# Optimization experiments

Measured on AMD Instinct MI355X. Metric: run time of the kernel, lower is better.

The kernel has to match this reference:

```python
import jax, jax.numpy as jnp
import numpy as np

NUM_ENT = 40000
NUM_REL = 100
EMBED_DIM = 256
FEAT_DIM = 768
BATCH = 32
SEQ_LEN = 3
MASK_POS = 2
EPS = 1e-12


def setup_inputs() -> dict:
    key = jax.random.key(0)
    k1, k2, k3, k4 = jax.random.split(key, 4)
    ent_pkl = jax.random.normal(k1, (NUM_ENT, FEAT_DIM), dtype=jnp.float32)
    other_emb = jax.random.normal(k2, (NUM_ENT + NUM_REL + 3 - NUM_ENT, EMBED_DIM), dtype=jnp.float32)
    proj_W = jax.random.normal(k3, (EMBED_DIM, FEAT_DIM), dtype=jnp.float32) * (1.0 / np.sqrt(FEAT_DIM))
    batch_input_ids = jax.random.randint(k4, (BATCH, SEQ_LEN), 0, NUM_ENT + NUM_REL + 3, dtype=jnp.int64)
    return {
        "ent_pkl": ent_pkl,
        "other_emb": other_emb,
        "proj_W": proj_W,
        "batch_input_ids": batch_input_ids,
        "batch_mask_position": MASK_POS,
    }


def reference(ent_pkl, other_emb, proj_W, batch_input_ids, batch_mask_position):
    # unity embeddings: [other[0], proj(ent_pkl), other[1:]] -> [num_ent+num_rel+3, d]
    ent_proj = ent_pkl @ proj_W.T  # Linear(feat_dim, embed_dim, bias=False)
    unity = jnp.concatenate([other_emb[:1], ent_proj, other_emb[1:]], axis=0)

    mp = int(batch_mask_position)
    # drop the masked slot, keep up to 3 tokens total -> [B, 2]
    query_input = jnp.concatenate(
        [batch_input_ids[:, :mp], batch_input_ids[:, mp + 1:3]], axis=1)
    query_emb = unity[query_input]  # [B, 2, d]
    # F.normalize(dim=-1): x / max(||x||_2, eps)
    norm = jnp.sqrt(jnp.sum(query_emb * query_emb, axis=-1, keepdims=True))
    query_emb = query_emb / jnp.maximum(norm, EPS)
    query_sum = jnp.sum(query_emb, axis=1)  # [B, d]

    E_embed = unity[:NUM_ENT + 1]  # [num_ent+1, d]
    # broadcast L1 distance: [B, num_ent+1]
    score = -jnp.sum(jnp.abs(query_sum[:, None, :] - E_embed[None, :, :]), axis=-1)
    return score
```

## Files before the change

kernel.cpp:

```cpp
#include <hip/hip_runtime.h>
#include <hip/hip_bf16.h>
#include <stdint.h>

#define NE 40000
#define FD 768
#define ED 256
#define NB 32
#define OUTC (NE + 1)

typedef __bf16 bf16x8 __attribute__((ext_vector_type(8)));
typedef float f32x4 __attribute__((ext_vector_type(4)));
typedef float f32x16 __attribute__((ext_vector_type(16)));
typedef _Float16 f16x2 __attribute__((ext_vector_type(2)));
typedef _Float16 f16x4 __attribute__((ext_vector_type(4)));

#define WS_QS 0
#define WS_N01 (32 * 1024)
#define WS_WB (96 * 1024)

__device__ __forceinline__ f16x2 pabs2(f16x2 d) {
    union { f16x2 h; unsigned u; } v; v.h = d; v.u &= 0x7FFF7FFFu; return v.h;
}

__device__ __forceinline__ void gload16(const void* g, void* l) {
    __builtin_amdgcn_global_load_lds(
        (const __attribute__((address_space(1))) unsigned int*)g,
        (__attribute__((address_space(3))) unsigned int*)l, 16, 0, 0);
}

__global__ __launch_bounds__(256) void prep_kernel(
    const float* __restrict__ ent_pkl, const float* __restrict__ W,
    const int* __restrict__ ids, const int* __restrict__ mpos,
    __bf16* __restrict__ Wf, float* __restrict__ n01_raw)
{
    __shared__ f32x4 xs4[FD / 4];
    const int bid = blockIdx.x;
    const int t = threadIdx.x;

    if (bid < 192) {
        const int i = bid * 1024 + t * 4;
        const int r = i / FD, c = i - r * FD;
        float4 v = *(const float4*)(W + i);
        __bf16 o[4] = {(__bf16)v.x, (__bf16)v.y, (__bf16)v.z, (__bf16)v.w};
        const int f = ((r >> 5) * 48 + (c >> 4)) * 64 + (r & 31) + ((c >> 3) & 1) * 32;
        *(ushort4*)(Wf + (size_t)f * 8 + (c & 7)) = *(const ushort4*)o;
        return;
    }

    const int sub = bid - 192;
    const int slot = sub >> 2;
    const int oq = sub & 3;
    const int b = slot >> 1, s = slot & 1;
    const int mp = mpos[0];
    const int col = (s < mp) ? s : s + 1;
    const bool wide = (ids[1] == 0 && ids[3] == 0 && ids[5] == 0);
    const int flat = b * 3 + col;
    const int idx = wide ? ids[flat * 2] : ids[flat];
    if (!(idx >= 1 && idx <= NE)) return;

    if (t < FD / 4) xs4[t] = ((const f32x4*)(ent_pkl + (size_t)(idx - 1) * FD))[t];
    __syncthreads();

    const int l = t & 63, wv = t >> 6;
    const f32x4 x0 = xs4[l], x1 = xs4[l + 64], x2 = xs4[l + 128];
    const int obase = oq * 64 + wv * 16;
#pragma unroll 2
    for (int i = 0; i < 16; ++i) {
        const int o = obase + i;
        const f32x4* wr = (const f32x4*)(W + (size_t)o * FD);
        f32x4 w0 = wr[l], w1 = wr[l + 64], w2 = wr[l + 128];
        float p = w0[0] * x0[0] + w0[1] * x0[1] + w0[2] * x0[2] + w0[3] * x0[3]
                + w1[0] * x1[0] + w1[1] * x1[1] + w1[2] * x1[2] + w1[3] * x1[3]
                + w2[0] * x2[0] + w2[1] * x2[1] + w2[2] * x2[2] + w2[3] * x2[3];
#pragma unroll
        for (int off = 32; off; off >>= 1) p += __shfl_xor(p, off, 64);
        if (l == 0) n01_raw[slot * ED + o] = p;
    }
}

__global__ __launch_bounds__(256) void qsum_kernel(
    const float* __restrict__ other_emb, const float* __restrict__ n01_raw,
    const int* __restrict__ ids, const int* __restrict__ mpos,
    _Float16* __restrict__ qh, float* __restrict__ out)
{
    __shared__ float red[4];
    __shared__ float nshare;
    const int b = blockIdx.x, t = threadIdx.x;
    const int mp = mpos[0];
    const bool wide = (ids[1] == 0 && ids[3] == 0 && ids[5] == 0);

    float q = 0.f;
#pragma unroll
    for (int s = 0; s < 2; ++s) {
        const int col = (s < mp) ? s : s + 1;
        const int flat = b * 3 + col;
        const int idx = wide ? ids[flat * 2] : ids[flat];
        float v;
        if (idx >= 1 && idx <= NE) v = n01_raw[(b * 2 + s) * ED + t];
        else if (idx == 0) v = other_emb[t];
        else v = other_emb[(size_t)(idx - NE) * ED + t];

        float ss = v * v;
#pragma unroll
        for (int o = 32; o > 0; o >>= 1) ss += __shfl_down(ss, o, 64);
        if ((t & 63) == 0) red[t >> 6] = ss;
        __syncthreads();
        if (t == 0) nshare = fmaxf(sqrtf(red[0] + red[1] + red[2] + red[3]), 1e-12f);
        __syncthreads();
        q += v / nshare;
        __syncthreads();
    }
    qh[b * ED + t] = (_Float16)q;

    float d = fabsf(q - other_emb[t]);
#pragma unroll
    for (int o = 32; o > 0; o >>= 1) d += __shfl_down(d, o, 64);
    if ((t & 63) == 0) red[t >> 6] = d;
    __syncthreads();
    if (t == 0) out[(size_t)b * OUTC] = -(red[0] + red[1] + red[2] + red[3]);
}

#define SP 256

__global__ __launch_bounds__(512, 6) void gemm_score_kernel(
    const float* __restrict__ ent_pkl, const __bf16* __restrict__ Wf,
    const _Float16* __restrict__ qh, float* __restrict__ out)
{
    __shared__ __align__(16) unsigned char smem[49152];
    float* Af = (float*)smem;
    _Float16* Sb = (_Float16*)smem;
    _Float16* qL = (_Float16*)(smem + 32768);

    const int t = threadIdx.x;
    const int l = t & 63;
    const int w = t >> 6;
    const int m31 = l & 31;
    const int dh = l >> 5;
    const int e0 = blockIdx.x * 64;

    f32x16 acc0, acc1;
#pragma unroll
    for (int i = 0; i < 16; ++i) { acc0[i] = 0.f; acc1[i] = 0.f; }

    int srow[6], slc[6];
#pragma unroll
    for (int j = 0; j < 6; ++j) {
        const int p = j * 512 + t;
        const int r = p / 48;
        srow[j] = r;
        slc[j] = (p - r * 48) ^ (r & 7);
    }

    const __bf16* bp = Wf + (size_t)w * 24576 + (size_t)l * 8;
    const int sw = m31 & 7;
    const float* a0base = Af + m31 * 192;
    const float* a1base = Af + (32 + m31) * 192;

    for (int q = 0; q < 4; ++q) {
        __syncthreads();
#pragma unroll
        for (int j = 0; j < 6; ++j) {
            gload16(ent_pkl + (size_t)(e0 + srow[j]) * FD + q * 192 + slc[j] * 4,
                    (float*)smem + (size_t)(j * 512 + t) * 4);
        }
        __syncthreads();
        const __bf16* bq = bp + (size_t)q * 12 * 512;
#pragma unroll 4
        for (int c = 0; c < 12; ++c) {
            bf16x8 bv = *(const bf16x8*)(bq + c * 512);
            const int u0 = 4 * c + 2 * dh;
            const int p0 = (u0 ^ sw) * 4, p1 = ((u0 + 1) ^ sw) * 4;
            f32x4 lo0 = *(const f32x4*)(a0base + p0);
            f32x4 hi0 = *(const f32x4*)(a0base + p1);
            f32x4 lo1 = *(const f32x4*)(a1base + p0);
            f32x4 hi1 = *(const f32x4*)(a1base + p1);
            bf16x8 a0, a1;
            a0[0] = (__bf16)lo0[0]; a0[1] = (__bf16)lo0[1]; a0[2] = (__bf16)lo0[2]; a0[3] = (__bf16)lo0[3];
            a0[4] = (__bf16)hi0[0]; a0[5] = (__bf16)hi0[1]; a0[6] = (__bf16)hi0[2]; a0[7] = (__bf16)hi0[3];
            a1[0] = (__bf16)lo1[0]; a1[1] = (__bf16)lo1[1]; a1[2] = (__bf16)lo1[2]; a1[3] = (__bf16)lo1[3];
            a1[4] = (__bf16)hi1[0]; a1[5] = (__bf16)hi1[1]; a1[6] = (__bf16)hi1[2]; a1[7] = (__bf16)hi1[3];
            acc0 = __builtin_amdgcn_mfma_f32_32x32x16_bf16(a0, bv, acc0, 0, 0, 0);
            acc1 = __builtin_amdgcn_mfma_f32_32x32x16_bf16(a1, bv, acc1, 0, 0, 0);
        }
    }

    __syncthreads();
    const int colg = 8 * w + (m31 >> 2);
    const int csub = m31 & 3;
#pragma unroll
    for (int r = 0; r < 16; ++r) {
        const int erow = (r & 3) + 8 * (r >> 2) + 4 * dh;
        const int ph = (((colg ^ (erow & 15)) << 2) | csub);
        Sb[erow * SP + ph] = (_Float16)acc0[r];
        Sb[(32 + erow) * SP + ph] = (_Float16)acc1[r];
    }
    {
        const uint4* qsrc = (const uint4*)qh;
        uint4* qdst = (uint4*)qL;
        qdst[t] = qsrc[t];
        qdst[t + 512] = qsrc[t + 512];
    }
    __syncthreads();

    const int wu = __builtin_amdgcn_readfirstlane(w);
    const f16x4* q0 = (const f16x4*)(qL + (size_t)(4 * wu + 0) * ED);
    const f16x4* q1 = (const f16x4*)(qL + (size_t)(4 * wu + 1) * ED);
    const f16x4* q2 = (const f16x4*)(qL + (size_t)(4 * wu + 2) * ED);
    const f16x4* q3 = (const f16x4*)(qL + (size_t)(4 * wu + 3) * ED);
    const int swl = l & 15;
    const _Float16* xbase = Sb + (size_t)l * SP;

    float s0 = 0.f, s1 = 0.f, s2 = 0.f, s3 = 0.f;
    for (int cb = 0; cb < 8; ++cb) {
        f16x2 t0 = {0, 0}, t1 = {0, 0}, t2 = {0, 0}, t3 = {0, 0};
#pragma unroll
        for (int ci = 0; ci < 8; ++ci) {
            const int c = cb * 8 + ci;
            f16x4 xv = *(const f16x4*)(xbase + ((c ^ swl) << 2));
            f16x2 xlo = __builtin_shufflevector(xv, xv, 0, 1);
            f16x2 xhi = __builtin_shufflevector(xv, xv, 2, 3);
            f16x4 qa = q0[c], qb = q1[c], qc = q2[c], qd = q3[c];
            t0 = t0 + pabs2(__builtin_shufflevector(qa, qa, 0, 1) - xlo);
            t0 = t0 + pabs2(__builtin_shufflevector(qa, qa, 2, 3) - xhi);
            t1 = t1 + pabs2(__builtin_shufflevector(qb, qb, 0, 1) - xlo);
            t1 = t1 + pabs2(__builtin_shufflevector(qb, qb, 2, 3) - xhi);
            t2 = t2 + pabs2(__builtin_shufflevector(qc, qc, 0, 1) - xlo);
            t2 = t2 + pabs2(__builtin_shufflevector(qc, qc, 2, 3) - xhi);
            t3 = t3 + pabs2(__builtin_shufflevector(qd, qd, 0, 1) - xlo);
            t3 = t3 + pabs2(__builtin_shufflevector(qd, qd, 2, 3) - xhi);
        }
        s0 += (float)t0[0] + (float)t0[1];
        s1 += (float)t1[0] + (float)t1[1];
        s2 += (float)t2[0] + (float)t2[1];
        s3 += (float)t3[0] + (float)t3[1];
    }
    float* ob = out + 1 + e0 + l;
    __builtin_nontemporal_store(-s0, ob + (size_t)(4 * wu + 0) * OUTC);
    __builtin_nontemporal_store(-s1, ob + (size_t)(4 * wu + 1) * OUTC);
    __builtin_nontemporal_store(-s2, ob + (size_t)(4 * wu + 2) * OUTC);
    __builtin_nontemporal_store(-s3, ob + (size_t)(4 * wu + 3) * OUTC);
}

extern "C" void kernel_launch(void* const* d_in, const int* in_sizes, int n_in,
                              void* d_out, int out_size, void* d_ws, size_t ws_size,
                              hipStream_t stream) {
    const float* ent_pkl = (const float*)d_in[0];
    const float* other_emb = (const float*)d_in[1];
    const float* proj_W = (const float*)d_in[2];
    const int* ids = (const int*)d_in[3];
    const int* mpos = (const int*)d_in[4];
    float* out = (float*)d_out;

    _Float16* qh = (_Float16*)((char*)d_ws + WS_QS);
    float* n01_raw = (float*)((char*)d_ws + WS_N01);
    __bf16* Wf = (__bf16*)((char*)d_ws + WS_WB);

    prep_kernel<<<448, 256, 0, stream>>>(ent_pkl, proj_W, ids, mpos, Wf, n01_raw);
    qsum_kernel<<<NB, 256, 0, stream>>>(other_emb, n01_raw, ids, mpos, qh, out);
    gemm_score_kernel<<<NE / 64, 512, 0, stream>>>(ent_pkl, Wf, qh, out);
}
```

Baseline: 245.4 us.

## Double-buffer bf16 A tiles in register-staged pipeline and restructure projection prep

The GEMM kernel now loads ent_pkl rows into registers and converts them to bf16 once per element before writing them into one of two ping-pong LDS buffers in MFMA fragment layout. The next K-slab's global loads are issued before the current slab's MFMAs, and it takes a single barrier per step instead of two around direct global-to-LDS loads. This removes the repeated fp32-to-bf16 conversions in the inner loop and halves LDS footprint per stage, at the cost of more register pressure and eight smaller K steps. The prep kernel's query-projection path is also rewritten so each thread computes one output dot product serially, with fewer blocks launched.

```diff
diff --git a/kernel.cpp b/kernel.cpp
--- a/kernel.cpp
+++ b/kernel.cpp
@@ -8,6 +8,7 @@
 #define NB 32
 #define OUTC (NE + 1)
 
+typedef __bf16 bf16x4 __attribute__((ext_vector_type(4)));
 typedef __bf16 bf16x8 __attribute__((ext_vector_type(8)));
 typedef float f32x4 __attribute__((ext_vector_type(4)));
 typedef float f32x16 __attribute__((ext_vector_type(16)));
@@ -22,18 +23,11 @@
     union { f16x2 h; unsigned u; } v; v.h = d; v.u &= 0x7FFF7FFFu; return v.h;
 }
 
-__device__ __forceinline__ void gload16(const void* g, void* l) {
-    __builtin_amdgcn_global_load_lds(
-        (const __attribute__((address_space(1))) unsigned int*)g,
-        (__attribute__((address_space(3))) unsigned int*)l, 16, 0, 0);
-}
-
 __global__ __launch_bounds__(256) void prep_kernel(
     const float* __restrict__ ent_pkl, const float* __restrict__ W,
     const int* __restrict__ ids, const int* __restrict__ mpos,
     __bf16* __restrict__ Wf, float* __restrict__ n01_raw)
 {
-    __shared__ f32x4 xs4[FD / 4];
     const int bid = blockIdx.x;
     const int t = threadIdx.x;
 
@@ -47,34 +41,36 @@
         return;
     }
 
-    const int sub = bid - 192;
-    const int slot = sub >> 2;
-    const int oq = sub & 3;
-    const int b = slot >> 1, s = slot & 1;
+    const int pb = bid - 192;
     const int mp = mpos[0];
-    const int col = (s < mp) ? s : s + 1;
     const bool wide = (ids[1] == 0 && ids[3] == 0 && ids[5] == 0);
-    const int flat = b * 3 + col;
-    const int idx = wide ? ids[flat * 2] : ids[flat];
-    if (!(idx >= 1 && idx <= NE)) return;
-
-    if (t < FD / 4) xs4[t] = ((const f32x4*)(ent_pkl + (size_t)(idx - 1) * FD))[t];
-    __syncthreads();
-
-    const int l = t & 63, wv = t >> 6;
-    const f32x4 x0 = xs4[l], x1 = xs4[l + 64], x2 = xs4[l + 128];
-    const int obase = oq * 64 + wv * 16;
-#pragma unroll 2
-    for (int i = 0; i < 16; ++i) {
-        const int o = obase + i;
-        const f32x4* wr = (const f32x4*)(W + (size_t)o * FD);
-        f32x4 w0 = wr[l], w1 = wr[l + 64], w2 = wr[l + 128];
-        float p = w0[0] * x0[0] + w0[1] * x0[1] + w0[2] * x0[2] + w0[3] * x0[3]
-                + w1[0] * x1[0] + w1[1] * x1[1] + w1[2] * x1[2] + w1[3] * x1[3]
-                + w2[0] * x2[0] + w2[1] * x2[1] + w2[2] * x2[2] + w2[3] * x2[3];
-#pragma unroll
-        for (int off = 32; off; off >>= 1) p += __shfl_xor(p, off, 64);
-        if (l == 0) n01_raw[slot * ED + o] = p;
+
+#pragma unroll
+    for (int sub = 0; sub < 2; ++sub) {
+        const int id = sub * 256 + t;
+        const int o = id & 7;
+        const int s = id >> 3;
+        const int b = s >> 1, sq = s & 1;
+        const int col = (sq < mp) ? sq : sq + 1;
+        const int flat = b * 3 + col;
+        const int idx = wide ? ids[flat * 2] : ids[flat];
+        if (!(idx >= 1 && idx <= NE)) continue;
+
+        const f32x4* wr = (const f32x4*)(W + (size_t)(pb * 8 + o) * FD);
+        const f32x4* xr = (const f32x4*)(ent_pkl + (size_t)(idx - 1) * FD);
+        float a0 = 0.f, a1 = 0.f, a2 = 0.f, a3 = 0.f;
+#pragma unroll 4
+        for (int k = 0; k < FD / 4; k += 4) {
+            f32x4 w0 = wr[k], x0 = xr[k];
+            f32x4 w1 = wr[k + 1], x1 = xr[k + 1];
+            f32x4 w2 = wr[k + 2], x2 = xr[k + 2];
+            f32x4 w3 = wr[k + 3], x3 = xr[k + 3];
+            a0 += w0[0]*x0[0] + w0[1]*x0[1] + w0[2]*x0[2] + w0[3]*x0[3];
+            a1 += w1[0]*x1[0] + w1[1]*x1[1] + w1[2]*x1[2] + w1[3]*x1[3];
+            a2 += w2[0]*x2[0] + w2[1]*x2[1] + w2[2]*x2[2] + w2[3]*x2[3];
+            a3 += w3[0]*x3[0] + w3[1]*x3[1] + w3[2]*x3[2] + w3[3]*x3[3];
+        }
+        n01_raw[s * ED + pb * 8 + o] = (a0 + a1) + (a2 + a3);
     }
 }
 
@@ -121,13 +117,25 @@
 }
 
 #define SP 256
+#define ABUF 12288
+
+__device__ __forceinline__ void write3(__bf16* B, const int* woff, const f32x4* st) {
+#pragma unroll
+    for (int j = 0; j < 3; ++j) {
+        bf16x4 v;
+        v[0] = (__bf16)st[j][0]; v[1] = (__bf16)st[j][1];
+        v[2] = (__bf16)st[j][2]; v[3] = (__bf16)st[j][3];
+        *(bf16x4*)((char*)B + woff[j]) = v;
+    }
+}
 
 __global__ __launch_bounds__(512, 6) void gemm_score_kernel(
     const float* __restrict__ ent_pkl, const __bf16* __restrict__ Wf,
     const _Float16* __restrict__ qh, float* __restrict__ out)
 {
     __shared__ __align__(16) unsigned char smem[49152];
-    float* Af = (float*)smem;
+    __bf16* A0 = (__bf16*)smem;
+    __bf16* A1 = (__bf16*)(smem + ABUF);
     _Float16* Sb = (_Float16*)smem;
     _Float16* qL = (_Float16*)(smem + 32768);
 
@@ -142,45 +150,47 @@
 #pragma unroll
     for (int i = 0; i < 16; ++i) { acc0[i] = 0.f; acc1[i] = 0.f; }
 
-    int srow[6], slc[6];
-#pragma unroll
-    for (int j = 0; j < 6; ++j) {
-        const int p = j * 512 + t;
-        const int r = p / 48;
-        srow[j] = r;
-        slc[j] = (p - r * 48) ^ (r & 7);
+    const int srow = t >> 3, sseg = t & 7;
+    const float* abase = ent_pkl + (size_t)(e0 + srow) * FD + sseg * 12;
+    int woff[3];
+#pragma unroll
+    for (int j = 0; j < 3; ++j) {
+        const int k0 = sseg * 12 + 4 * j;
+        const int unit = ((k0 >> 4) * 2 + ((k0 >> 3) & 1)) * 64 + srow;
+        woff[j] = unit * 16 + (k0 & 7) * 2;
     }
 
     const __bf16* bp = Wf + (size_t)w * 24576 + (size_t)l * 8;
-    const int sw = m31 & 7;
-    const float* a0base = Af + m31 * 192;
-    const float* a1base = Af + (32 + m31) * 192;
-
-    for (int q = 0; q < 4; ++q) {
-        __syncthreads();
-#pragma unroll
-        for (int j = 0; j < 6; ++j) {
-            gload16(ent_pkl + (size_t)(e0 + srow[j]) * FD + q * 192 + slc[j] * 4,
-                    (float*)smem + (size_t)(j * 512 + t) * 4);
-        }
-        __syncthreads();
-        const __bf16* bq = bp + (size_t)q * 12 * 512;
-#pragma unroll 4
-        for (int c = 0; c < 12; ++c) {
+
+    f32x4 st[3];
+    st[0] = *(const f32x4*)(abase + 0);
+    st[1] = *(const f32x4*)(abase + 4);
+    st[2] = *(const f32x4*)(abase + 8);
+    write3(A0, woff, st);
+    __syncthreads();
+
+    for (int p = 0; p < 8; ++p) {
+        const __bf16* Ab = (p & 1) ? A1 : A0;
+        __bf16* An = (p & 1) ? A0 : A1;
+        if (p < 7) {
+            const float* np = abase + (p + 1) * 96;
+            st[0] = *(const f32x4*)(np + 0);
+            st[1] = *(const f32x4*)(np + 4);
+            st[2] = *(const f32x4*)(np + 8);
+        }
+        const __bf16* bq = bp + (size_t)p * 6 * 512;
+#pragma unroll
+        for (int c = 0; c < 6; ++c) {
             bf16x8 bv = *(const bf16x8*)(bq + c * 512);
-            const int u0 = 4 * c + 2 * dh;
-            const int p0 = (u0 ^ sw) * 4, p1 = ((u0 + 1) ^ sw) * 4;
-            f32x4 lo0 = *(const f32x4*)(a0base + p0);
-            f32x4 hi0 = *(const f32x4*)(a0base + p1);
-            f32x4 lo1 = *(const f32x4*)(a1base + p0);
-            f32x4 hi1 = *(const f32x4*)(a1base + p1);
-            bf16x8 a0, a1;
-            a0[0] = (__bf16)lo0[0]; a0[1] = (__bf16)lo0[1]; a0[2] = (__bf16)lo0[2]; a0[3] = (__bf16)lo0[3];
-            a0[4] = (__bf16)hi0[0]; a0[5] = (__bf16)hi0[1]; a0[6] = (__bf16)hi0[2]; a0[7] = (__bf16)hi0[3];
-            a1[0] = (__bf16)lo1[0]; a1[1] = (__bf16)lo1[1]; a1[2] = (__bf16)lo1[2]; a1[3] = (__bf16)lo1[3];
-            a1[4] = (__bf16)hi1[0]; a1[5] = (__bf16)hi1[1]; a1[6] = (__bf16)hi1[2]; a1[7] = (__bf16)hi1[3];
+            const __bf16* fa = Ab + ((c * 2 + dh) * 64 + m31) * 8;
+            bf16x8 a0 = *(const bf16x8*)(fa);
+            bf16x8 a1 = *(const bf16x8*)(fa + 256);
             acc0 = __builtin_amdgcn_mfma_f32_32x32x16_bf16(a0, bv, acc0, 0, 0, 0);
             acc1 = __builtin_amdgcn_mfma_f32_32x32x16_bf16(a1, bv, acc1, 0, 0, 0);
+        }
+        if (p < 7) {
+            write3(An, woff, st);
+            __syncthreads();
         }
     }
 
@@ -255,7 +265,7 @@
     float* n01_raw = (float*)((char*)d_ws + WS_N01);
     __bf16* Wf = (__bf16*)((char*)d_ws + WS_WB);
 
-    prep_kernel<<<448, 256, 0, stream>>>(ent_pkl, proj_W, ids, mpos, Wf, n01_raw);
+    prep_kernel<<<224, 256, 0, stream>>>(ent_pkl, proj_W, ids, mpos, Wf, n01_raw);
     qsum_kernel<<<NB, 256, 0, stream>>>(other_emb, n01_raw, ids, mpos, qh, out);
     gemm_score_kernel<<<NE / 64, 512, 0, stream>>>(ent_pkl, Wf, qh, out);
 }
```

Result: slower. 270.2 us (+10.1%).

## Software-pipeline GEMM A loads with 4-stage LDS ring and MFMA prep projection

Applied to the files above, without the earlier changes.

The main gemm_score kernel now streams ent_pkl tiles in 64-column phases through a 4-buffer LDS ring. Global-to-LDS loads are issued three phases ahead with explicit vmcnt waits, and the bf16 W fragments are double-buffered in registers. This replaces the previous load-all, sync, then compute quarters. The prep kernel's 64 query-row projection is also rewritten as a single-block MFMA GEMM using the same pipeline, replacing 256 blocks of dot-product reductions. This raises LDS to 64KB, so occupancy drops to 4 blocks per CU, and hand-tuned waitcnt counts risk subtle hazards.

```diff
diff --git a/kernel.cpp b/kernel.cpp
--- a/kernel.cpp
+++ b/kernel.cpp
@@ -22,23 +22,30 @@
     union { f16x2 h; unsigned u; } v; v.h = d; v.u &= 0x7FFF7FFFu; return v.h;
 }
 
+__device__ __forceinline__ bf16x8 cvt8(f32x4 lo, f32x4 hi) {
+    bf16x8 v;
+    v[0] = (__bf16)lo[0]; v[1] = (__bf16)lo[1]; v[2] = (__bf16)lo[2]; v[3] = (__bf16)lo[3];
+    v[4] = (__bf16)hi[0]; v[5] = (__bf16)hi[1]; v[6] = (__bf16)hi[2]; v[7] = (__bf16)hi[3];
+    return v;
+}
+
 __device__ __forceinline__ void gload16(const void* g, void* l) {
     __builtin_amdgcn_global_load_lds(
         (const __attribute__((address_space(1))) unsigned int*)g,
         (__attribute__((address_space(3))) unsigned int*)l, 16, 0, 0);
 }
 
-__global__ __launch_bounds__(256) void prep_kernel(
+
+__global__ __launch_bounds__(512) void prep_kernel(
     const float* __restrict__ ent_pkl, const float* __restrict__ W,
     const int* __restrict__ ids, const int* __restrict__ mpos,
     __bf16* __restrict__ Wf, float* __restrict__ n01_raw)
 {
-    __shared__ f32x4 xs4[FD / 4];
-    const int bid = blockIdx.x;
+    __shared__ __align__(16) unsigned char smem[65536];
     const int t = threadIdx.x;
 
-    if (bid < 192) {
-        const int i = bid * 1024 + t * 4;
+    if (blockIdx.x < 96) {
+        const int i = blockIdx.x * 2048 + t * 4;
         const int r = i / FD, c = i - r * FD;
         float4 v = *(const float4*)(W + i);
         __bf16 o[4] = {(__bf16)v.x, (__bf16)v.y, (__bf16)v.z, (__bf16)v.w};
@@ -47,34 +54,77 @@
         return;
     }
 
-    const int sub = bid - 192;
-    const int slot = sub >> 2;
-    const int oq = sub & 3;
-    const int b = slot >> 1, s = slot & 1;
+    const int l = t & 63;
+    const int w = t >> 6;
+    const int m31 = l & 31;
+    const int dh = l >> 5;
+    const int sw = m31 & 15;
     const int mp = mpos[0];
-    const int col = (s < mp) ? s : s + 1;
     const bool wide = (ids[1] == 0 && ids[3] == 0 && ids[5] == 0);
-    const int flat = b * 3 + col;
-    const int idx = wide ? ids[flat * 2] : ids[flat];
-    if (!(idx >= 1 && idx <= NE)) return;
-
-    if (t < FD / 4) xs4[t] = ((const f32x4*)(ent_pkl + (size_t)(idx - 1) * FD))[t];
-    __syncthreads();
-
-    const int l = t & 63, wv = t >> 6;
-    const f32x4 x0 = xs4[l], x1 = xs4[l + 64], x2 = xs4[l + 128];
-    const int obase = oq * 64 + wv * 16;
-#pragma unroll 2
-    for (int i = 0; i < 16; ++i) {
-        const int o = obase + i;
-        const f32x4* wr = (const f32x4*)(W + (size_t)o * FD);
-        f32x4 w0 = wr[l], w1 = wr[l + 64], w2 = wr[l + 128];
-        float p = w0[0] * x0[0] + w0[1] * x0[1] + w0[2] * x0[2] + w0[3] * x0[3]
-                + w1[0] * x1[0] + w1[1] * x1[1] + w1[2] * x1[2] + w1[3] * x1[3]
-                + w2[0] * x2[0] + w2[1] * x2[1] + w2[2] * x2[2] + w2[3] * x2[3];
-#pragma unroll
-        for (int off = 32; off; off >>= 1) p += __shfl_xor(p, off, 64);
-        if (l == 0) n01_raw[slot * ED + o] = p;
+
+    const int r1 = t >> 4;
+    const int goff = ((t & 15) ^ (r1 & 15)) * 4;
+    int rowA, rowB;
+    {
+        int s = r1;
+        int b = s >> 1, sq = s & 1;
+        int col = (sq < mp) ? sq : sq + 1;
+        int flat = b * 3 + col;
+        int idx = wide ? ids[flat * 2] : ids[flat];
+        rowA = (idx >= 1 && idx <= NE) ? idx - 1 : 0;
+        s = r1 + 32;
+        b = s >> 1; sq = s & 1;
+        col = (sq < mp) ? sq : sq + 1;
+        flat = b * 3 + col;
+        idx = wide ? ids[flat * 2] : ids[flat];
+        rowB = (idx >= 1 && idx <= NE) ? idx - 1 : 0;
+    }
+    const float* ab1 = ent_pkl + (size_t)rowA * FD + goff;
+    const float* ab2 = ent_pkl + (size_t)rowB * FD + goff;
+    const float* Wr = W + (size_t)(32 * w + m31) * FD + 8 * dh;
+
+    f32x16 acc0, acc1;
+#pragma unroll
+    for (int i = 0; i < 16; ++i) { acc0[i] = 0.f; acc1[i] = 0.f; }
+
+#define P_ISSUE(P) { char* lb = (char*)smem + ((P) & 3) * 16384 + t * 16; \
+        gload16(ab1 + (P) * 64, lb); gload16(ab2 + (P) * 64, lb + 8192); }
+
+#define P_PHASE(P, NW, DOISS) \
+    asm volatile("s_waitcnt vmcnt(" #NW ")" ::: "memory"); \
+    __builtin_amdgcn_s_barrier(); \
+    __builtin_amdgcn_sched_barrier(0); \
+    { \
+        f32x4 wv[8]; \
+        _Pragma("unroll") for (int c2 = 0; c2 < 4; ++c2) { \
+            wv[2 * c2]     = *(const f32x4*)(Wr + 16 * (4 * (P) + c2)); \
+            wv[2 * c2 + 1] = *(const f32x4*)(Wr + 16 * (4 * (P) + c2) + 4); \
+        } \
+        __builtin_amdgcn_sched_barrier(0); \
+        if (DOISS) P_ISSUE((P) + 3); \
+        const char* Ab = (const char*)smem + ((P) & 3) * 16384; \
+        _Pragma("unroll") for (int c2 = 0; c2 < 4; ++c2) { \
+            const int u0 = (4 * c2 + 2 * dh) ^ sw; \
+            const char* pa = Ab + (m31 * 16 + u0) * 16; \
+            const char* pb = Ab + (m31 * 16 + (u0 ^ 1)) * 16; \
+            f32x4 lo0 = *(const f32x4*)pa,          hi0 = *(const f32x4*)pb; \
+            f32x4 lo1 = *(const f32x4*)(pa + 8192), hi1 = *(const f32x4*)(pb + 8192); \
+            bf16x8 bv = cvt8(wv[2 * c2], wv[2 * c2 + 1]); \
+            acc0 = __builtin_amdgcn_mfma_f32_32x32x16_bf16(cvt8(lo0, hi0), bv, acc0, 0, 0, 0); \
+            acc1 = __builtin_amdgcn_mfma_f32_32x32x16_bf16(cvt8(lo1, hi1), bv, acc1, 0, 0, 0); \
+        } \
+    }
+
+    P_ISSUE(0); P_ISSUE(1); P_ISSUE(2);
+    P_PHASE(0, 4, 1)  P_PHASE(1, 8, 1)  P_PHASE(2, 8, 1)  P_PHASE(3, 8, 1)
+    P_PHASE(4, 8, 1)  P_PHASE(5, 8, 1)  P_PHASE(6, 8, 1)  P_PHASE(7, 8, 1)
+    P_PHASE(8, 8, 1)  P_PHASE(9, 8, 0)  P_PHASE(10, 8, 0) P_PHASE(11, 8, 0)
+
+#pragma unroll
+    for (int r = 0; r < 16; ++r) {
+        const int erow = (r & 3) + 8 * (r >> 2) + 4 * dh;
+        n01_raw[erow * ED + 32 * w + m31] = acc0[r];
+        n01_raw[(32 + erow) * ED + 32 * w + m31] = acc1[r];
     }
 }
 
@@ -122,12 +172,11 @@
 
 #define SP 256
 
-__global__ __launch_bounds__(512, 6) void gemm_score_kernel(
+__global__ __launch_bounds__(512, 4) void gemm_score_kernel(
     const float* __restrict__ ent_pkl, const __bf16* __restrict__ Wf,
     const _Float16* __restrict__ qh, float* __restrict__ out)
 {
-    __shared__ __align__(16) unsigned char smem[49152];
-    float* Af = (float*)smem;
+    __shared__ __align__(16) unsigned char smem[65536];
     _Float16* Sb = (_Float16*)smem;
     _Float16* qL = (_Float16*)(smem + 32768);
 
@@ -136,53 +185,55 @@
     const int w = t >> 6;
     const int m31 = l & 31;
     const int dh = l >> 5;
+    const int sw = m31 & 15;
     const int e0 = blockIdx.x * 64;
 
     f32x16 acc0, acc1;
 #pragma unroll
     for (int i = 0; i < 16; ++i) { acc0[i] = 0.f; acc1[i] = 0.f; }
 
-    int srow[6], slc[6];
-#pragma unroll
-    for (int j = 0; j < 6; ++j) {
-        const int p = j * 512 + t;
-        const int r = p / 48;
-        srow[j] = r;
-        slc[j] = (p - r * 48) ^ (r & 7);
-    }
-
+    const int r1 = t >> 4;
+    const int goff = ((t & 15) ^ (r1 & 15)) * 4;
+    const float* ab1 = ent_pkl + (size_t)(e0 + r1) * FD + goff;
+    const float* ab2 = ent_pkl + (size_t)(e0 + r1 + 32) * FD + goff;
     const __bf16* bp = Wf + (size_t)w * 24576 + (size_t)l * 8;
-    const int sw = m31 & 7;
-    const float* a0base = Af + m31 * 192;
-    const float* a1base = Af + (32 + m31) * 192;
-
-    for (int q = 0; q < 4; ++q) {
-        __syncthreads();
-#pragma unroll
-        for (int j = 0; j < 6; ++j) {
-            gload16(ent_pkl + (size_t)(e0 + srow[j]) * FD + q * 192 + slc[j] * 4,
-                    (float*)smem + (size_t)(j * 512 + t) * 4);
-        }
-        __syncthreads();
-        const __bf16* bq = bp + (size_t)q * 12 * 512;
-#pragma unroll 4
-        for (int c = 0; c < 12; ++c) {
-            bf16x8 bv = *(const bf16x8*)(bq + c * 512);
-            const int u0 = 4 * c + 2 * dh;
-            const int p0 = (u0 ^ sw) * 4, p1 = ((u0 + 1) ^ sw) * 4;
-            f32x4 lo0 = *(const f32x4*)(a0base + p0);
-            f32x4 hi0 = *(const f32x4*)(a0base + p1);
-            f32x4 lo1 = *(const f32x4*)(a1base + p0);
-            f32x4 hi1 = *(const f32x4*)(a1base + p1);
-            bf16x8 a0, a1;
-            a0[0] = (__bf16)lo0[0]; a0[1] = (__bf16)lo0[1]; a0[2] = (__bf16)lo0[2]; a0[3] = (__bf16)lo0[3];
-            a0[4] = (__bf16)hi0[0]; a0[5] = (__bf16)hi0[1]; a0[6] = (__bf16)hi0[2]; a0[7] = (__bf16)hi0[3];
-            a1[0] = (__bf16)lo1[0]; a1[1] = (__bf16)lo1[1]; a1[2] = (__bf16)lo1[2]; a1[3] = (__bf16)lo1[3];
-            a1[4] = (__bf16)hi1[0]; a1[5] = (__bf16)hi1[1]; a1[6] = (__bf16)hi1[2]; a1[7] = (__bf16)hi1[3];
-            acc0 = __builtin_amdgcn_mfma_f32_32x32x16_bf16(a0, bv, acc0, 0, 0, 0);
-            acc1 = __builtin_amdgcn_mfma_f32_32x32x16_bf16(a1, bv, acc1, 0, 0, 0);
-        }
-    }
+
+    bf16x8 bvA[4], bvB[4];
+
+#define G_ISSUE(P) { char* lb = (char*)smem + ((P) & 3) * 16384 + t * 16; \
+        gload16(ab1 + (P) * 64, lb); gload16(ab2 + (P) * 64, lb + 8192); }
+
+#define G_PHASE(P, NW, BUSE, BNEXT, DOISS, DOLOAD) \
+    asm volatile("s_waitcnt vmcnt(" #NW ")" ::: "memory"); \
+    __builtin_amdgcn_s_barrier(); \
+    __builtin_amdgcn_sched_barrier(0); \
+    if (DOLOAD) { _Pragma("unroll") for (int c2 = 0; c2 < 4; ++c2) \
+        BNEXT[c2] = *(const bf16x8*)(bp + (size_t)(4 * ((P) + 1) + c2) * 512); } \
+    __builtin_amdgcn_sched_barrier(0); \
+    if (DOISS) G_ISSUE((P) + 3); \
+    { \
+        const char* Ab = (const char*)smem + ((P) & 3) * 16384; \
+        _Pragma("unroll") for (int c2 = 0; c2 < 4; ++c2) { \
+            const int u0 = (4 * c2 + 2 * dh) ^ sw; \
+            const char* pa = Ab + (m31 * 16 + u0) * 16; \
+            const char* pb = Ab + (m31 * 16 + (u0 ^ 1)) * 16; \
+            f32x4 lo0 = *(const f32x4*)pa,          hi0 = *(const f32x4*)pb; \
+            f32x4 lo1 = *(const f32x4*)(pa + 8192), hi1 = *(const f32x4*)(pb + 8192); \
+            acc0 = __builtin_amdgcn_mfma_f32_32x32x16_bf16(cvt8(lo0, hi0), BUSE[c2], acc0, 0, 0, 0); \
+            acc1 = __builtin_amdgcn_mfma_f32_32x32x16_bf16(cvt8(lo1, hi1), BUSE[c2], acc1, 0, 0, 0); \
+        } \
+    }
+
+    G_ISSUE(0); G_ISSUE(1); G_ISSUE(2);
+#pragma unroll
+    for (int c2 = 0; c2 < 4; ++c2) bvA[c2] = *(const bf16x8*)(bp + (size_t)c2 * 512);
+
+    G_PHASE(0, 8, bvA, bvB, 1, 1)   G_PHASE(1, 8, bvB, bvA, 1, 1)
+    G_PHASE(2, 8, bvA, bvB, 1, 1)   G_PHASE(3, 8, bvB, bvA, 1, 1)
+    G_PHASE(4, 8, bvA, bvB, 1, 1)   G_PHASE(5, 8, bvB, bvA, 1, 1)
+    G_PHASE(6, 8, bvA, bvB, 1, 1)   G_PHASE(7, 8, bvB, bvA, 1, 1)
+    G_PHASE(8, 8, bvA, bvB, 1, 1)   G_PHASE(9, 8, bvB, bvA, 0, 1)
+    G_PHASE(10, 6, bvA, bvB, 0, 1)  G_PHASE(11, 4, bvB, bvA, 0, 0)
 
     __syncthreads();
     const int colg = 8 * w + (m31 >> 2);
@@ -255,7 +306,7 @@
     float* n01_raw = (float*)((char*)d_ws + WS_N01);
     __bf16* Wf = (__bf16*)((char*)d_ws + WS_WB);
 
-    prep_kernel<<<448, 256, 0, stream>>>(ent_pkl, proj_W, ids, mpos, Wf, n01_raw);
+    prep_kernel<<<97, 512, 0, stream>>>(ent_pkl, proj_W, ids, mpos, Wf, n01_raw);
     qsum_kernel<<<NB, 256, 0, stream>>>(other_emb, n01_raw, ids, mpos, qh, out);
     gemm_score_kernel<<<NE / 64, 512, 0, stream>>>(ent_pkl, Wf, qh, out);
 }
```

Result: slower. 267.2 us (+8.9%).
